# Kernel optimization log

Hardware: AMD Instinct MI355X
Metric: run time of the kernel (lower is better)

## Reference

```python
import jax, jax.numpy as jnp
import numpy as np

B, H, W, C = 1, 64, 64, 768
HEADS = 12
HD = C // HEADS  # 64


def setup_inputs() -> dict:
    key = jax.random.key(0)
    ks = jax.random.split(key, 11)
    s = 0.02
    return {
        "hidden_states": jax.random.normal(ks[0], (B, H, W, C), jnp.float32),
        "w_q": jax.random.normal(ks[1], (C, C), jnp.float32) * s,
        "b_q": jnp.zeros((C,), jnp.float32),
        "w_k": jax.random.normal(ks[2], (C, C), jnp.float32) * s,
        "b_k": jnp.zeros((C,), jnp.float32),
        "w_v": jax.random.normal(ks[3], (C, C), jnp.float32) * s,
        "b_v": jnp.zeros((C,), jnp.float32),
        "w_o": jax.random.normal(ks[4], (C, C), jnp.float32) * s,
        "b_o": jnp.zeros((C,), jnp.float32),
        "rel_pos_h": jax.random.normal(ks[5], (2 * H - 1, HD), jnp.float32) * s,
        "rel_pos_w": jax.random.normal(ks[6], (2 * W - 1, HD), jnp.float32) * s,
    }


def _get_rel_pos(q_size, k_size, rel_pos):
    # q_size == k_size here, so no interpolation branch; pure gather.
    coords = jnp.arange(q_size)[:, None] - jnp.arange(k_size)[None, :] + (k_size - 1)
    return rel_pos[coords]  # (q_size, k_size, head_dim)


def reference(hidden_states, w_q, b_q, w_k, b_k, w_v, b_v, w_o, b_o, rel_pos_h, rel_pos_w):
    b, h, w, c = hidden_states.shape
    hd = c // HEADS

    def proj(wm, bm):
        y = hidden_states @ wm.T + bm  # (b,h,w,c)
        return y.reshape(b, h * w, HEADS, hd).transpose(0, 2, 1, 3)  # (b,heads,hw,hd)

    q = proj(w_q, b_q)
    k = proj(w_k, b_k)
    v = proj(w_v, b_v)

    # decomposed relative position bias (per head-dim query)
    Rh = _get_rel_pos(h, h, rel_pos_h)  # (h,h,hd)
    Rw = _get_rel_pos(w, w, rel_pos_w)  # (w,w,hd)
    qr = q.reshape(b, HEADS, h, w, hd)
    rel_h = jnp.einsum('bnhwc,hkc->bnhwk', qr, Rh)  # (b,heads,h,w,h)
    rel_w = jnp.einsum('bnhwc,wkc->bnhwk', qr, Rw)  # (b,heads,h,w,w)
    attn_bias = (rel_h[..., :, None] + rel_w[..., None, :]).reshape(b, HEADS, h * w, h * w)

    scale = hd ** -0.5
    scores = jnp.einsum('bnqd,bnkd->bnqk', q, k) * scale + attn_bias
    attn = jax.nn.softmax(scores, axis=-1)
    out = jnp.einsum('bnqk,bnkd->bnqd', attn, v)  # (b,heads,hw,hd)
    out = out.transpose(0, 2, 1, 3).reshape(b, h, w, c)
    return out @ w_o.T + b_o
```

## Files before the change

kernel.cpp:

```cpp
#include <hip/hip_runtime.h>


typedef __attribute__((ext_vector_type(8))) short bf16x8;
typedef __attribute__((ext_vector_type(4))) float f32x4;
typedef __attribute__((ext_vector_type(4))) short s16x4;
typedef __attribute__((ext_vector_type(2))) unsigned int u32x2;
typedef __attribute__((ext_vector_type(4))) unsigned int u32x4;

__device__ __forceinline__ float b2f(unsigned short h) {
    union { unsigned int u; float f; } v; v.u = ((unsigned int)h) << 16; return v.f;
}
__device__ __forceinline__ unsigned short f2b(float f) {
    union { float f; unsigned int u; } v; v.f = f;
    unsigned int r = v.u + 0x7FFFu + ((v.u >> 16) & 1u);
    return (unsigned short)(r >> 16);
}
__device__ __forceinline__ void gl_lds16(const void* g, void* l) {
    __builtin_amdgcn_global_load_lds(
        (const __attribute__((address_space(1))) void*)g,
        (__attribute__((address_space(3))) void*)l, 16, 0, 0);
}

__global__ __launch_bounds__(256) void cvt_bf16(
        const float* __restrict__ hs, const float* __restrict__ wq,
        const float* __restrict__ wk, const float* __restrict__ wv,
        const float* __restrict__ wo, const float* __restrict__ rph,
        const float* __restrict__ rpw, unsigned short* __restrict__ dst) {
    const int idx = blockIdx.x * 256 + threadIdx.x;
    if (idx >= 1380320) return;
    const float* src;
    int off;
    if      (idx < 786432)  { src = hs;  off = idx; }
    else if (idx < 933888)  { src = wq;  off = idx - 786432; }
    else if (idx < 1081344) { src = wk;  off = idx - 933888; }
    else if (idx < 1228800) { src = wv;  off = idx - 1081344; }
    else if (idx < 1376256) { src = wo;  off = idx - 1228800; }
    else if (idx < 1378288) { src = rph; off = idx - 1376256; }
    else                    { src = rpw; off = idx - 1378288; }
    const float4 v = ((const float4*)src)[off];
    s16x4 o;
    o[0] = (short)f2b(v.x); o[1] = (short)f2b(v.y);
    o[2] = (short)f2b(v.z); o[3] = (short)f2b(v.w);
    *(s16x4*)(dst + (size_t)idx * 4) = o;
}

__launch_bounds__(256, 3)
__global__ void qkv128(const unsigned short* __restrict__ X,
                       const unsigned short* __restrict__ Wq,
                       const unsigned short* __restrict__ Wk,
                       const unsigned short* __restrict__ Wv,
                       const float* __restrict__ bq,
                       const float* __restrict__ bk,
                       const float* __restrict__ bv,
                       unsigned short* __restrict__ qb,
                       unsigned short* __restrict__ kb,
                       unsigned short* __restrict__ vtb) {
    __shared__ __align__(16) unsigned short sarena[16384];
    const int tid = threadIdx.x, lane = tid & 63, w = tid >> 6;
    const int r = lane & 15, quad = lane >> 4;
    const int lin = blockIdx.x;
    const int wk576 = (lin & 7) * 72 + (lin >> 3);
    const int nt = wk576 % 6, mt = (wk576 / 6) & 31, z = wk576 / 192;
    const unsigned short* W  = (z == 0) ? Wq : (z == 1) ? Wk : Wv;
    const float*          Bv = (z == 0) ? bq : (z == 1) ? bk : bv;
    unsigned short*     outp = (z == 0) ? qb : (z == 1) ? kb : vtb;
    const float qsc = (z == 0) ? 0.18033688f : 1.0f;

    const int c0 = w * 64 + lane, c1 = c0 + 256;
    const unsigned short* xs0 = X + (mt * 128 + (c0 & 127)) * 768 + (c0 >> 7) * 8;
    const unsigned short* xs1 = X + (mt * 128 + (c1 & 127)) * 768 + (c1 >> 7) * 8;
    const unsigned short* ws0 = W + (nt * 128 + (c0 & 127)) * 768 + (c0 >> 7) * 8;
    const unsigned short* ws1 = W + (nt * 128 + (c1 & 127)) * 768 + (c1 >> 7) * 8;

    gl_lds16(xs0, &sarena[w * 512]);
    gl_lds16(xs1, &sarena[2048 + w * 512]);
    gl_lds16(ws0, &sarena[4096 + w * 512]);
    gl_lds16(ws1, &sarena[4096 + 2048 + w * 512]);
    __syncthreads();

    const int wr = (w & 1) * 64, wc = (w >> 1) * 64;
    f32x4 acc[4][4] = {};
    int cur = 0;
#pragma unroll 2
    for (int kt = 0; kt < 24; ++kt) {
        if (kt < 23) {
            const int nx = (cur ^ 1) * 8192;
            gl_lds16(xs0 + (kt + 1) * 32, &sarena[nx + w * 512]);
            gl_lds16(xs1 + (kt + 1) * 32, &sarena[nx + 2048 + w * 512]);
            gl_lds16(ws0 + (kt + 1) * 32, &sarena[nx + 4096 + w * 512]);
            gl_lds16(ws1 + (kt + 1) * 32, &sarena[nx + 4096 + 2048 + w * 512]);
        }
        const unsigned short* ab = &sarena[cur * 8192];
        const unsigned short* bb = ab + 4096;
        bf16x8 af[4], bfr[4];
#pragma unroll
        for (int i = 0; i < 4; ++i)
            af[i] = *(const bf16x8*)&ab[(quad * 128 + wr + i * 16 + r) * 8];
#pragma unroll
        for (int j = 0; j < 4; ++j)
            bfr[j] = *(const bf16x8*)&bb[(quad * 128 + wc + j * 16 + r) * 8];
#pragma unroll
        for (int i = 0; i < 4; ++i)
#pragma unroll
            for (int j = 0; j < 4; ++j)
                acc[i][j] = __builtin_amdgcn_mfma_f32_16x16x32_bf16(af[i], bfr[j], acc[i][j], 0, 0, 0);
        __syncthreads();
        cur ^= 1;
    }
    if (z < 2) {
#pragma unroll
        for (int j = 0; j < 4; ++j) {
            const int n = nt * 128 + wc + j * 16 + r;
            const float bias = Bv[n];
            const int nhi = n >> 6, nlo = n & 63;
#pragma unroll
            for (int i = 0; i < 4; ++i) {
#pragma unroll
                for (int reg = 0; reg < 4; ++reg) {
                    const int m = mt * 128 + wr + i * 16 + quad * 4 + reg;
                    outp[(nhi * 4096 + m) * 64 + nlo] = f2b((acc[i][j][reg] + bias) * qsc);
                }
            }
        }
    } else {
#pragma unroll
        for (int pass = 0; pass < 2; ++pass) {
            if ((w >> 1) == pass) {
#pragma unroll
                for (int j = 0; j < 4; ++j) {
                    const int n_l = j * 16 + r;
                    const float bias = Bv[nt * 128 + pass * 64 + n_l];
                    const int sw = (n_l & 7) << 4;
#pragma unroll
                    for (int reg = 0; reg < 4; ++reg) {
                        const int tokb = (wr + (quad * 4 + reg) * 4) ^ sw;
                        u32x2 d2;
                        d2.x = (unsigned int)f2b(acc[0][j][reg] + bias)
                             | ((unsigned int)f2b(acc[1][j][reg] + bias) << 16);
                        d2.y = (unsigned int)f2b(acc[2][j][reg] + bias)
                             | ((unsigned int)f2b(acc[3][j][reg] + bias) << 16);
                        *(u32x2*)&sarena[n_l * 128 + tokb] = d2;
                    }
                }
            }
            __syncthreads();
#pragma unroll
            for (int c = 0; c < 4; ++c) {
                const int u = c * 256 + tid;
                const int n_l = u >> 4, g = u & 15;
                const int phys = n_l * 128 + ((g * 8) ^ ((n_l & 7) << 4));
                bf16x8 val = *(const bf16x8*)&sarena[phys];
                *(bf16x8*)&outp[(size_t)(nt * 128 + pass * 64 + n_l) * 4096
                                + mt * 128 + g * 8] = val;
            }
            __syncthreads();
        }
    }
}

__launch_bounds__(256, 3)
__global__ void out128(const unsigned short* __restrict__ X,
                       const unsigned short* __restrict__ W,
                       const float* __restrict__ Bv,
                       float* __restrict__ out) {
    __shared__ __align__(16) unsigned short sarena[16384];
    const int tid = threadIdx.x, lane = tid & 63, w = tid >> 6;
    const int r = lane & 15, quad = lane >> 4;
    const int lin = blockIdx.x;
    const int wk192 = (lin & 7) * 24 + (lin >> 3);
    const int nt = wk192 % 6, mt = wk192 / 6;

    const int c0 = w * 64 + lane, c1 = c0 + 256;
    const unsigned short* xs0 = X + (mt * 128 + (c0 & 127)) * 768 + (c0 >> 7) * 8;
    const unsigned short* xs1 = X + (mt * 128 + (c1 & 127)) * 768 + (c1 >> 7) * 8;
    const unsigned short* ws0 = W + (nt * 128 + (c0 & 127)) * 768 + (c0 >> 7) * 8;
    const unsigned short* ws1 = W + (nt * 128 + (c1 & 127)) * 768 + (c1 >> 7) * 8;

    gl_lds16(xs0, &sarena[w * 512]);
    gl_lds16(xs1, &sarena[2048 + w * 512]);
    gl_lds16(ws0, &sarena[4096 + w * 512]);
    gl_lds16(ws1, &sarena[4096 + 2048 + w * 512]);
    __syncthreads();

    const int wr = (w & 1) * 64, wc = (w >> 1) * 64;
    f32x4 acc[4][4] = {};
    int cur = 0;
#pragma unroll 2
    for (int kt = 0; kt < 24; ++kt) {
        if (kt < 23) {
            const int nx = (cur ^ 1) * 8192;
            gl_lds16(xs0 + (kt + 1) * 32, &sarena[nx + w * 512]);
            gl_lds16(xs1 + (kt + 1) * 32, &sarena[nx + 2048 + w * 512]);
            gl_lds16(ws0 + (kt + 1) * 32, &sarena[nx + 4096 + w * 512]);
            gl_lds16(ws1 + (kt + 1) * 32, &sarena[nx + 4096 + 2048 + w * 512]);
        }
        const unsigned short* ab = &sarena[cur * 8192];
        const unsigned short* bb = ab + 4096;
        bf16x8 af[4], bfr[4];
#pragma unroll
        for (int i = 0; i < 4; ++i)
            af[i] = *(const bf16x8*)&ab[(quad * 128 + wr + i * 16 + r) * 8];
#pragma unroll
        for (int j = 0; j < 4; ++j)
            bfr[j] = *(const bf16x8*)&bb[(quad * 128 + wc + j * 16 + r) * 8];
#pragma unroll
        for (int i = 0; i < 4; ++i)
#pragma unroll
            for (int j = 0; j < 4; ++j)
                acc[i][j] = __builtin_amdgcn_mfma_f32_16x16x32_bf16(af[i], bfr[j], acc[i][j], 0, 0, 0);
        __syncthreads();
        cur ^= 1;
    }
#pragma unroll
    for (int j = 0; j < 4; ++j) {
        const int n = nt * 128 + wc + j * 16 + r;
        const float bias = Bv[n];
#pragma unroll
        for (int i = 0; i < 4; ++i) {
#pragma unroll
            for (int reg = 0; reg < 4; ++reg) {
                const int m = mt * 128 + wr + i * 16 + quad * 4 + reg;
                out[m * 768 + n] = acc[i][j][reg] + bias;
            }
        }
    }
}

__launch_bounds__(256, 4)
__global__ void relk(const unsigned short* __restrict__ qbuf,
                     const unsigned short* __restrict__ rph,
                     const unsigned short* __restrict__ rpw,
                     unsigned short* __restrict__ rh,
                     unsigned short* __restrict__ rw) {
    __shared__ __align__(16) unsigned short abuf[8 * 64 * 8];
    __shared__ __align__(16) unsigned short bbuf[8 * 64 * 8];
    const int tid = threadIdx.x;
    const int lane = tid & 63, w = tid >> 6;
    const int r = lane & 15, quad = lane >> 4;
    const int a = blockIdx.x, h = blockIdx.y, mode = blockIdx.z;
    const unsigned short* rp = mode ? rpw : rph;
    const float osc = 8.0f;

#pragma unroll
    for (int gg = 0; gg < 2; ++gg) {
        const int g = w * 2 + gg;
        const int arow = mode ? (h * 4096 + lane * 64 + a) : (h * 4096 + a * 64 + lane);
        gl_lds16(qbuf + arow * 64 + g * 8, &abuf[g * 512]);
        const int bidx = a - lane + 63;
        gl_lds16(rp + bidx * 64 + g * 8, &bbuf[g * 512]);
    }
    __syncthreads();

    f32x4 acc[4] = {};
#pragma unroll
    for (int s = 0; s < 2; ++s) {
        bf16x8 af = *(const bf16x8*)&abuf[((s * 4 + quad) * 64 + w * 16 + r) * 8];
#pragma unroll
        for (int j = 0; j < 4; ++j) {
            bf16x8 bfr = *(const bf16x8*)&bbuf[((s * 4 + quad) * 64 + j * 16 + r) * 8];
            acc[j] = __builtin_amdgcn_mfma_f32_16x16x32_bf16(af, bfr, acc[j], 0, 0, 0);
        }
    }
    unsigned short* out = mode ? rw : rh;
#pragma unroll
    for (int j = 0; j < 4; ++j) {
#pragma unroll
        for (int reg = 0; reg < 4; ++reg) {
            const int m = w * 16 + quad * 4 + reg, n = j * 16 + r;
            const int t = mode ? (h * 4096 + m * 64 + a) : (h * 4096 + a * 64 + m);
            out[t * 64 + n] = f2b(acc[j][reg] * osc);
        }
    }
}

__launch_bounds__(256, 3)
__global__ void attn2(const unsigned short* __restrict__ qbuf,
                      const unsigned short* __restrict__ kbuf,
                      const unsigned short* __restrict__ vtbuf,
                      const unsigned short* __restrict__ rhb,
                      const unsigned short* __restrict__ rwb,
                      float* __restrict__ po, float* __restrict__ lp) {
    __shared__ __align__(16) unsigned short skb[4096];
    __shared__ __align__(16) unsigned short svb[4096];
    __shared__ __align__(16) unsigned short spb[9216];
    __shared__ __align__(16) unsigned short srh[4096];
    const int tid = threadIdx.x;
    const int lane = tid & 63, w = tid >> 6;
    const int r = lane & 15, quad = lane >> 4;
    const int bid = blockIdx.x;
    const int wk768 = (bid & 7) * 96 + (bid >> 3);
    const int h = wk768 >> 6, sp = (wk768 >> 5) & 1, qt = wk768 & 31;

#pragma unroll
    for (int i = 0; i < 2; ++i) {
        const int ql = (w & 1) * 64 + lane;
        gl_lds16(rhb + (h * 4096 + qt * 128 + ql) * 64 + (sp * 4 + i * 2 + (w >> 1)) * 8,
                 &srh[(i * 256 + w * 64) * 8]);
    }
    const unsigned short* ksrc = kbuf + (size_t)(h * 4096 + lane) * 64 + w * 16;
    const unsigned short* vsrc = vtbuf + (size_t)(h * 64 + lane) * 4096 + w * 16;
    u32x4 kp0, kp1, vp0, vp1;
    {
        const int t0 = sp * 32;
        kp0 = *(const u32x4*)(ksrc + (size_t)t0 * 4096);
        kp1 = *(const u32x4*)(ksrc + (size_t)t0 * 4096 + 8);
        vp0 = *(const u32x4*)(vsrc + t0 * 64);
        vp1 = *(const u32x4*)(vsrc + t0 * 64 + 8);
    }
    bf16x8 qf[2][2];
#pragma unroll
    for (int g = 0; g < 2; ++g) {
        const unsigned short* qrow =
            qbuf + (h * 4096 + qt * 128 + g * 64 + w * 16 + r) * 64;
        qf[g][0] = *(const bf16x8*)(qrow + quad * 8);
        qf[g][1] = *(const bf16x8*)(qrow + 32 + quad * 8);
    }
    float rwL[2][4][4];
#pragma unroll
    for (int g = 0; g < 2; ++g) {
        const unsigned short* rwrow = rwb + (h * 4096 + qt * 128 + g * 64) * 64;
#pragma unroll
        for (int reg = 0; reg < 4; ++reg) {
            const int ql = w * 16 + quad * 4 + reg;
#pragma unroll
            for (int j = 0; j < 4; ++j)
                rwL[g][j][reg] = b2f(rwrow[ql * 64 + j * 16 + r]);
        }
    }
    bf16x8 onesf;
#pragma unroll
    for (int i = 0; i < 8; ++i) onesf[i] = (short)0x3F80;

    f32x4 lacc[2] = {};
    f32x4 oacc[2][4] = {};
    __syncthreads();
    *(u32x4*)&skb[(w * 128 + lane) * 8]      = kp0;
    *(u32x4*)&skb[(w * 128 + 64 + lane) * 8] = kp1;
    *(u32x4*)&svb[(w * 128 + lane) * 8]      = vp0;
    *(u32x4*)&svb[(w * 128 + 64 + lane) * 8] = vp1;
    __syncthreads();

    for (int tl = 0; tl < 32; ++tl) {
        const int t = sp * 32 + tl;
        if (tl < 31) {
            kp0 = *(const u32x4*)(ksrc + (size_t)(t + 1) * 4096);
            kp1 = *(const u32x4*)(ksrc + (size_t)(t + 1) * 4096 + 8);
            vp0 = *(const u32x4*)(vsrc + (t + 1) * 64);
            vp1 = *(const u32x4*)(vsrc + (t + 1) * 64 + 8);
        }
        float rh2f[8];
#pragma unroll
        for (int i = 0; i < 8; ++i)
            rh2f[i] = b2f(srh[((tl >> 3) * 128 + (i >> 2) * 64 + w * 16
                               + quad * 4 + (i & 3)) * 8 + (t & 7)]);
        f32x4 s0[4], s1[4];
#pragma unroll
        for (int j = 0; j < 4; ++j)
#pragma unroll
            for (int reg = 0; reg < 4; ++reg) {
                s0[j][reg] = rh2f[reg]     + rwL[0][j][reg];
                s1[j][reg] = rh2f[4 + reg] + rwL[1][j][reg];
            }
        __builtin_amdgcn_s_setprio(1);
#pragma unroll
        for (int s2 = 0; s2 < 2; ++s2) {
#pragma unroll
            for (int j = 0; j < 4; ++j) {
                bf16x8 kf = *(const bf16x8*)&skb[((s2 * 4 + quad) * 64 + j * 16 + r) * 8];
                s0[j] = __builtin_amdgcn_mfma_f32_16x16x32_bf16(qf[0][s2], kf, s0[j], 0, 0, 0);
                s1[j] = __builtin_amdgcn_mfma_f32_16x16x32_bf16(qf[1][s2], kf, s1[j], 0, 0, 0);
            }
        }
        __builtin_amdgcn_s_setprio(0);
#pragma unroll
        for (int g = 0; g < 2; ++g) {
#pragma unroll
            for (int reg = 0; reg < 4; ++reg) {
                unsigned int u[4];
#pragma unroll
                for (int j = 0; j < 4; ++j) {
                    const float p = __builtin_amdgcn_exp2f(g ? s1[j][reg] : s0[j][reg]);
                    union { float f; unsigned int q; } cv; cv.f = p;
                    u[j] = cv.q;
                }
                u32x2 d;
                d.x = __builtin_amdgcn_perm(u[1], u[0], 0x07060302);
                d.y = __builtin_amdgcn_perm(u[3], u[2], 0x07060302);
                *(u32x2*)&spb[g * 4608 + w * 1152 + (quad * 4 + reg) * 72 + r * 4] = d;
            }
        }
        __builtin_amdgcn_s_setprio(1);
#pragma unroll
        for (int s = 0; s < 2; ++s) {
            bf16x8 pf0 = *(const bf16x8*)&spb[w * 1152 + r * 72 + s * 32 + quad * 8];
            bf16x8 pf1 = *(const bf16x8*)&spb[4608 + w * 1152 + r * 72 + s * 32 + quad * 8];
            lacc[0] = __builtin_amdgcn_mfma_f32_16x16x32_bf16(pf0, onesf, lacc[0], 0, 0, 0);
            lacc[1] = __builtin_amdgcn_mfma_f32_16x16x32_bf16(pf1, onesf, lacc[1], 0, 0, 0);
#pragma unroll
            for (int j = 0; j < 4; ++j) {
                bf16x8 vf = *(const bf16x8*)&svb[((s * 4 + quad) * 64 + j * 16 + r) * 8];
                oacc[0][j] = __builtin_amdgcn_mfma_f32_16x16x32_bf16(pf0, vf, oacc[0][j], 0, 0, 0);
                oacc[1][j] = __builtin_amdgcn_mfma_f32_16x16x32_bf16(pf1, vf, oacc[1][j], 0, 0, 0);
            }
        }
        __builtin_amdgcn_s_setprio(0);

        __syncthreads();
        if (tl < 31) {
            *(u32x4*)&skb[(w * 128 + lane) * 8]      = kp0;
            *(u32x4*)&skb[(w * 128 + 64 + lane) * 8] = kp1;
            *(u32x4*)&svb[(w * 128 + lane) * 8]      = vp0;
            *(u32x4*)&svb[(w * 128 + 64 + lane) * 8] = vp1;
        }
        __syncthreads();
    }
    const size_t pbase = ((size_t)(sp * 12 + h) * 4096 + qt * 128);
#pragma unroll
    for (int g = 0; g < 2; ++g) {
        const int qrow = g * 64 + w * 16 + quad * 4;
#pragma unroll
        for (int reg = 0; reg < 4; ++reg) {
#pragma unroll
            for (int j = 0; j < 4; ++j)
                po[(pbase + qrow + reg) * 64 + j * 16 + r] = oacc[g][j][reg];
            if (r == 0) lp[pbase + qrow + reg] = lacc[g][reg];
        }
    }
}

__global__ __launch_bounds__(256) void combine(const float* __restrict__ po,
                                               const float* __restrict__ lp,
                                               unsigned short* __restrict__ ab) {
    const unsigned int idx = blockIdx.x * 256 + threadIdx.x;
    const unsigned int tok = idx / 96u;
    const unsigned int part = idx - tok * 96u;
    const int c = part * 8, h = c >> 6, d = c & 63;
    const float* p0 = po + ((size_t)h * 4096 + tok) * 64 + d;
    const float* p1 = po + ((size_t)(12 + h) * 4096 + tok) * 64 + d;
    const float inv = 1.f / (lp[h * 4096 + tok] + lp[(12 + h) * 4096 + tok]);
    const float4 a0 = *(const float4*)p0, b0 = *(const float4*)(p0 + 4);
    const float4 a1 = *(const float4*)p1, b1 = *(const float4*)(p1 + 4);
    s16x4 o0, o1;
    o0[0] = (short)f2b((a0.x + a1.x) * inv); o0[1] = (short)f2b((a0.y + a1.y) * inv);
    o0[2] = (short)f2b((a0.z + a1.z) * inv); o0[3] = (short)f2b((a0.w + a1.w) * inv);
    o1[0] = (short)f2b((b0.x + b1.x) * inv); o1[1] = (short)f2b((b0.y + b1.y) * inv);
    o1[2] = (short)f2b((b0.z + b1.z) * inv); o1[3] = (short)f2b((b0.w + b1.w) * inv);
    unsigned short* dst = ab + (size_t)tok * 768 + c;
    *(s16x4*)dst = o0;
    *(s16x4*)(dst + 4) = o1;
}

extern "C" void kernel_launch(void* const* d_in, const int* in_sizes, int n_in,
                              void* d_out, int out_size, void* d_ws, size_t ws_size,
                              hipStream_t stream) {
    const float* hs  = (const float*)d_in[0];
    const float* wq  = (const float*)d_in[1];
    const float* bq  = (const float*)d_in[2];
    const float* wk  = (const float*)d_in[3];
    const float* bk  = (const float*)d_in[4];
    const float* wv  = (const float*)d_in[5];
    const float* bv  = (const float*)d_in[6];
    const float* wo  = (const float*)d_in[7];
    const float* bo  = (const float*)d_in[8];
    const float* rph = (const float*)d_in[9];
    const float* rpw = (const float*)d_in[10];

    unsigned short* ws = (unsigned short*)d_ws;
    const int HS = 3145728, WN = 589824, RP = 8128;
    const int HB = 12 * 4096 * 64;
    unsigned short* hsb  = ws;
    unsigned short* wqb  = hsb  + HS;
    unsigned short* wkb  = wqb  + WN;
    unsigned short* wvb  = wkb  + WN;
    unsigned short* wob  = wvb  + WN;
    unsigned short* rphb = wob  + WN;
    unsigned short* rpwb = rphb + RP;
    unsigned short* qb   = rpwb + RP;
    unsigned short* kb   = qb   + HB;
    unsigned short* vtb  = kb   + HB;
    unsigned short* rhb  = vtb  + HB;
    unsigned short* rwb  = rhb  + HB;
    unsigned short* ab   = rwb  + HB;
    float* po = (float*)(ab + HB);
    float* lp = po + 2 * 12 * 4096 * 64;

    cvt_bf16<<<dim3((1380320 + 255) / 256), 256, 0, stream>>>(
        hs, wq, wk, wv, wo, rph, rpw, hsb);
    qkv128<<<dim3(576), 256, 0, stream>>>(
        hsb, wqb, wkb, wvb, bq, bk, bv, qb, kb, vtb);
    relk<<<dim3(64, 12, 2), 256, 0, stream>>>(qb, rphb, rpwb, rhb, rwb);
    attn2<<<dim3(768), 256, 0, stream>>>(qb, kb, vtb, rhb, rwb, po, lp);
    combine<<<dim3(1536), 256, 0, stream>>>(po, lp, ab);
    out128<<<dim3(192), 256, 0, stream>>>(ab, wob, bo, (float*)d_out);
}
```

Measured before the change: 227.1 us.

## Double-buffer K/V tiles in LDS and reuse a single P staging buffer

K and V tiles now go into two alternating LDS buffers, so the next tile is written while the current one is read. This drops one of the two block-wide barriers per iteration. The P staging buffer is halved by processing the two 64-row query groups one after another, each writing P and then doing its PV MFMAs. That keeps total LDS use about the same, but it serialises the two groups' PV work and adds an extra LDS write/read round trip on each group's P data.

```diff
diff --git a/kernel.cpp b/kernel.cpp
--- a/kernel.cpp
+++ b/kernel.cpp
@@ -280,9 +280,9 @@
                       const unsigned short* __restrict__ rhb,
                       const unsigned short* __restrict__ rwb,
                       float* __restrict__ po, float* __restrict__ lp) {
-    __shared__ __align__(16) unsigned short skb[4096];
-    __shared__ __align__(16) unsigned short svb[4096];
-    __shared__ __align__(16) unsigned short spb[9216];
+    __shared__ __align__(16) unsigned short skb[2][4096];
+    __shared__ __align__(16) unsigned short svb[2][4096];
+    __shared__ __align__(16) unsigned short spb[4608];
     __shared__ __align__(16) unsigned short srh[4096];
     const int tid = threadIdx.x;
     const int lane = tid & 63, w = tid >> 6;
@@ -333,13 +333,14 @@
 
     f32x4 lacc[2] = {};
     f32x4 oacc[2][4] = {};
+    *(u32x4*)&skb[0][(w * 128 + lane) * 8]      = kp0;
+    *(u32x4*)&skb[0][(w * 128 + 64 + lane) * 8] = kp1;
+    *(u32x4*)&svb[0][(w * 128 + lane) * 8]      = vp0;
+    *(u32x4*)&svb[0][(w * 128 + 64 + lane) * 8] = vp1;
     __syncthreads();
-    *(u32x4*)&skb[(w * 128 + lane) * 8]      = kp0;
-    *(u32x4*)&skb[(w * 128 + 64 + lane) * 8] = kp1;
-    *(u32x4*)&svb[(w * 128 + lane) * 8]      = vp0;
-    *(u32x4*)&svb[(w * 128 + 64 + lane) * 8] = vp1;
-    __syncthreads();
-
+
+    int cur = 0;
+#pragma unroll 2
     for (int tl = 0; tl < 32; ++tl) {
         const int t = sp * 32 + tl;
         if (tl < 31) {
@@ -366,7 +367,7 @@
         for (int s2 = 0; s2 < 2; ++s2) {
 #pragma unroll
             for (int j = 0; j < 4; ++j) {
-                bf16x8 kf = *(const bf16x8*)&skb[((s2 * 4 + quad) * 64 + j * 16 + r) * 8];
+                bf16x8 kf = *(const bf16x8*)&skb[cur][((s2 * 4 + quad) * 64 + j * 16 + r) * 8];
                 s0[j] = __builtin_amdgcn_mfma_f32_16x16x32_bf16(qf[0][s2], kf, s0[j], 0, 0, 0);
                 s1[j] = __builtin_amdgcn_mfma_f32_16x16x32_bf16(qf[1][s2], kf, s1[j], 0, 0, 0);
             }
@@ -386,33 +387,29 @@
                 u32x2 d;
                 d.x = __builtin_amdgcn_perm(u[1], u[0], 0x07060302);
                 d.y = __builtin_amdgcn_perm(u[3], u[2], 0x07060302);
-                *(u32x2*)&spb[g * 4608 + w * 1152 + (quad * 4 + reg) * 72 + r * 4] = d;
-            }
-        }
-        __builtin_amdgcn_s_setprio(1);
-#pragma unroll
-        for (int s = 0; s < 2; ++s) {
-            bf16x8 pf0 = *(const bf16x8*)&spb[w * 1152 + r * 72 + s * 32 + quad * 8];
-            bf16x8 pf1 = *(const bf16x8*)&spb[4608 + w * 1152 + r * 72 + s * 32 + quad * 8];
-            lacc[0] = __builtin_amdgcn_mfma_f32_16x16x32_bf16(pf0, onesf, lacc[0], 0, 0, 0);
-            lacc[1] = __builtin_amdgcn_mfma_f32_16x16x32_bf16(pf1, onesf, lacc[1], 0, 0, 0);
-#pragma unroll
-            for (int j = 0; j < 4; ++j) {
-                bf16x8 vf = *(const bf16x8*)&svb[((s * 4 + quad) * 64 + j * 16 + r) * 8];
-                oacc[0][j] = __builtin_amdgcn_mfma_f32_16x16x32_bf16(pf0, vf, oacc[0][j], 0, 0, 0);
-                oacc[1][j] = __builtin_amdgcn_mfma_f32_16x16x32_bf16(pf1, vf, oacc[1][j], 0, 0, 0);
-            }
-        }
-        __builtin_amdgcn_s_setprio(0);
-
+                *(u32x2*)&spb[w * 1152 + (quad * 4 + reg) * 72 + r * 4] = d;
+            }
+            __builtin_amdgcn_s_setprio(1);
+#pragma unroll
+            for (int s = 0; s < 2; ++s) {
+                bf16x8 pf = *(const bf16x8*)&spb[w * 1152 + r * 72 + s * 32 + quad * 8];
+                lacc[g] = __builtin_amdgcn_mfma_f32_16x16x32_bf16(pf, onesf, lacc[g], 0, 0, 0);
+#pragma unroll
+                for (int j = 0; j < 4; ++j) {
+                    bf16x8 vf = *(const bf16x8*)&svb[cur][((s * 4 + quad) * 64 + j * 16 + r) * 8];
+                    oacc[g][j] = __builtin_amdgcn_mfma_f32_16x16x32_bf16(pf, vf, oacc[g][j], 0, 0, 0);
+                }
+            }
+            __builtin_amdgcn_s_setprio(0);
+        }
+        if (tl < 31) {
+            *(u32x4*)&skb[cur ^ 1][(w * 128 + lane) * 8]      = kp0;
+            *(u32x4*)&skb[cur ^ 1][(w * 128 + 64 + lane) * 8] = kp1;
+            *(u32x4*)&svb[cur ^ 1][(w * 128 + lane) * 8]      = vp0;
+            *(u32x4*)&svb[cur ^ 1][(w * 128 + 64 + lane) * 8] = vp1;
+        }
         __syncthreads();
-        if (tl < 31) {
-            *(u32x4*)&skb[(w * 128 + lane) * 8]      = kp0;
-            *(u32x4*)&skb[(w * 128 + 64 + lane) * 8] = kp1;
-            *(u32x4*)&svb[(w * 128 + lane) * 8]      = vp0;
-            *(u32x4*)&svb[(w * 128 + 64 + lane) * 8] = vp1;
-        }
-        __syncthreads();
+        cur ^= 1;
     }
     const size_t pbase = ((size_t)(sp * 12 + h) * 4096 + qt * 128);
 #pragma unroll
```

New measurement: 301.1 us. 1.33x slower.
